# Kernel tuning notes

Measured on AMD Instinct MI355X. Metric: run time of the kernel, lower is better.

Reference implementation:

```python
import jax, jax.numpy as jnp
import numpy as np

EPS = 1e-5

def rmsnorm(x):
    # BitLinear pre-norm (no learnable scale), per BitNet b1.58 reference impl
    return x * jax.lax.rsqrt(jnp.mean(x * x, axis=-1, keepdims=True) + EPS)

def act_quant(x):
    # per-token absmax 8-bit quantization with straight-through estimator
    scale = 127.0 / jnp.clip(jnp.max(jnp.abs(x), axis=-1, keepdims=True), 1e-5)
    q = jnp.clip(jnp.round(x * scale), -128.0, 127.0) / scale
    return x + jax.lax.stop_gradient(q - x)

def weight_quant(w):
    # absmean ternary quantization {-1,0,1} with STE
    scale = 1.0 / jnp.clip(jnp.mean(jnp.abs(w)), 1e-5)
    q = jnp.clip(jnp.round(w * scale), -1.0, 1.0) / scale
    return w + jax.lax.stop_gradient(q - w)

def bitlinear(x, w, b):
    # x: [b, s, d_in], w: [d_out, d_in] (torch Linear layout), b: [d_out]
    xq = act_quant(rmsnorm(x))
    wq = weight_quant(w)
    return jnp.einsum('bsd,fd->bsf', xq, wq) + b

def setup_inputs() -> dict:
    key = jax.random.key(0)
    k0, k1, k2 = jax.random.split(key, 3)
    B, S, D, F = 2, 8192, 1024, 4096  # inner_dim = dim * mult = 4096
    x = jax.random.normal(k0, (B, S, D), dtype=jnp.float32)
    w1 = jax.random.normal(k1, (F, D), dtype=jnp.float32) * (1.0 / np.sqrt(D))
    b1 = jnp.zeros((F,), dtype=jnp.float32)
    w2 = jax.random.normal(k2, (D, F), dtype=jnp.float32) * (1.0 / np.sqrt(F))
    b2 = jnp.zeros((D,), dtype=jnp.float32)
    return {"x": x, "w1": w1, "b1": b1, "w2": w2, "b2": b2}

def reference(x, w1, b1, w2, b2):
    h = bitlinear(x, w1, b1)
    h = jax.nn.gelu(h, approximate=False)  # nn.GELU() default is exact
    # post_act_ln=False -> no LayerNorm; dropout p=0.0 -> identity
    return bitlinear(h, w2, b2)
```

## Files before the change

### kernel.cpp

```cpp
#include <hip/hip_runtime.h>
#include <hip/hip_bf16.h>
#include <stdint.h>

typedef int i32x4 __attribute__((ext_vector_type(4)));

__device__ __forceinline__ float blo(unsigned int u) {
  unsigned int v = u << 16; float f; __builtin_memcpy(&f, &v, 4); return f;
}
__device__ __forceinline__ float bhi(unsigned int u) {
  unsigned int v = u & 0xffff0000u; float f; __builtin_memcpy(&f, &v, 4); return f;
}
__device__ __forceinline__ int pack4q(float a, float b, float c, float d, float qm) {
  int i0 = (int)rintf(a * qm) & 255;
  int i1 = (int)rintf(b * qm) & 255;
  int i2 = (int)rintf(c * qm) & 255;
  int i3 = (int)rintf(d * qm) & 255;
  return i0 | (i1 << 8) | (i2 << 16) | (i3 << 24);
}

__device__ __forceinline__ float fast_gelu(float v) {
  float u = v * 0.70710678118654752f;
  float s = fabsf(u);
  float den = fmaf(0.3275911f, s, 1.0f);
  float t;
  asm("v_rcp_f32 %0, %1" : "=v"(t) : "v"(den));
  float p = t * fmaf(t, fmaf(t, fmaf(t, fmaf(t, 1.061405429f, -1.453152027f),
                                     1.421413741f), -0.284496736f), 0.254829592f);
  float e = fmaf(-p, __expf(-u * u), 1.0f);
  float er = copysignf(e, u);
  return 0.5f * v * (1.0f + er);
}

__global__ void k_reduce_abs2(const float* __restrict__ w1, const float* __restrict__ w2,
                              long n4, float* __restrict__ partials) {
  const int half = gridDim.x >> 1;
  const float* w = (blockIdx.x < half) ? w1 : w2;
  int b = (blockIdx.x < half) ? blockIdx.x : blockIdx.x - half;
  const float4* wv = (const float4*)w;
  float s = 0.0f;
  long stride = (long)half * blockDim.x;
  for (long i = (long)b * blockDim.x + threadIdx.x; i < n4; i += stride) {
    float4 v = wv[i];
    s += fabsf(v.x) + fabsf(v.y) + fabsf(v.z) + fabsf(v.w);
  }
  #pragma unroll
  for (int off = 32; off; off >>= 1) s += __shfl_down(s, off);
  __shared__ float sw[4];
  if ((threadIdx.x & 63) == 0) sw[threadIdx.x >> 6] = s;
  __syncthreads();
  if (threadIdx.x == 0) partials[blockIdx.x] = sw[0] + sw[1] + sw[2] + sw[3];
}

__global__ void k_quant_w2(const float* __restrict__ w1, char* __restrict__ wq1,
                           const float* __restrict__ w2, char* __restrict__ wq2,
                           long n4, const float* __restrict__ partials,
                           float* __restrict__ scales, float invW) {
  const int half = gridDim.x >> 1;
  const bool first = blockIdx.x < half;
  int t = threadIdx.x;
  float p = partials[(first ? 0 : 256) + t];
  #pragma unroll
  for (int off = 32; off; off >>= 1) p += __shfl_down(p, off);
  __shared__ float a[4];
  if ((t & 63) == 0) a[t >> 6] = p;
  __syncthreads();
  float sc = fmaxf((a[0] + a[1] + a[2] + a[3]) * invW, 1e-5f);
  if (t == 0 && (blockIdx.x == 0 || blockIdx.x == half)) scales[first ? 0 : 1] = sc;
  float s = 1.0f / sc;
  const float* w = first ? w1 : w2;
  char* wq = first ? wq1 : wq2;
  int b = first ? blockIdx.x : blockIdx.x - half;
  const float4* wv = (const float4*)w;
  int* qv = (int*)wq;
  long stride = (long)half * blockDim.x;
  for (long i = (long)b * blockDim.x + t; i < n4; i += stride) {
    float4 v = wv[i];
    int b0 = (int)fminf(fmaxf(rintf(v.x * s), -1.0f), 1.0f) & 255;
    int b1 = (int)fminf(fmaxf(rintf(v.y * s), -1.0f), 1.0f) & 255;
    int b2 = (int)fminf(fmaxf(rintf(v.z * s), -1.0f), 1.0f) & 255;
    int b3 = (int)fminf(fmaxf(rintf(v.w * s), -1.0f), 1.0f) & 255;
    qv[i] = b0 | (b1 << 8) | (b2 << 16) | (b3 << 24);
  }
}

__global__ void k_actq_x(const float* __restrict__ x, char* __restrict__ xq,
                         float* __restrict__ alpha) {
  const int D = 1024;
  size_t t = blockIdx.x;
  int tid = threadIdx.x;
  const float4* row = (const float4*)(x + t * (size_t)D);
  float4 v = row[tid];
  float ss = v.x*v.x + v.y*v.y + v.z*v.z + v.w*v.w;
  float am = fmaxf(fmaxf(fabsf(v.x), fabsf(v.y)), fmaxf(fabsf(v.z), fabsf(v.w)));
  #pragma unroll
  for (int off = 32; off; off >>= 1) {
    ss += __shfl_down(ss, off);
    am = fmaxf(am, __shfl_down(am, off));
  }
  __shared__ float s_ss[4], s_am[4];
  if ((tid & 63) == 0) { s_ss[tid >> 6] = ss; s_am[tid >> 6] = am; }
  __syncthreads();
  ss = s_ss[0] + s_ss[1] + s_ss[2] + s_ss[3];
  am = fmaxf(fmaxf(s_am[0], s_am[1]), fmaxf(s_am[2], s_am[3]));
  float rms = rsqrtf(ss * (1.0f / D) + 1e-5f);
  float a   = fmaxf(am * rms, 1e-5f);
  float qs  = 127.0f / a;
  if (tid == 0) alpha[t] = a * (1.0f / 127.0f);
  int b0 = (int)fminf(fmaxf(rintf((v.x * rms) * qs), -128.0f), 127.0f) & 255;
  int b1 = (int)fminf(fmaxf(rintf((v.y * rms) * qs), -128.0f), 127.0f) & 255;
  int b2 = (int)fminf(fmaxf(rintf((v.z * rms) * qs), -128.0f), 127.0f) & 255;
  int b3 = (int)fminf(fmaxf(rintf((v.w * rms) * qs), -128.0f), 127.0f) & 255;
  ((int*)xq)[t * 256 + tid] = b0 | (b1 << 8) | (b2 << 16) | (b3 << 24);
}

__global__ void k_actq_h(__hip_bfloat16* __restrict__ h, float* __restrict__ alpha) {
  const int F = 4096;
  size_t t = blockIdx.x;
  int tid = threadIdx.x;
  char* rb = (char*)(h + t * (size_t)F);
  const uint4* row = (const uint4*)rb;
  uint4 u0 = row[tid], u1 = row[tid + 256];
  unsigned int uu[8] = {u0.x, u0.y, u0.z, u0.w, u1.x, u1.y, u1.z, u1.w};
  float ss = 0.0f, am = 0.0f;
  #pragma unroll
  for (int i = 0; i < 8; i++) {
    float f0 = blo(uu[i]), f1 = bhi(uu[i]);
    ss += f0 * f0 + f1 * f1;
    am = fmaxf(am, fmaxf(fabsf(f0), fabsf(f1)));
  }
  #pragma unroll
  for (int off = 32; off; off >>= 1) {
    ss += __shfl_down(ss, off);
    am = fmaxf(am, __shfl_down(am, off));
  }
  __shared__ float s_ss[4], s_am[4];
  if ((tid & 63) == 0) { s_ss[tid >> 6] = ss; s_am[tid >> 6] = am; }
  __syncthreads();
  ss = s_ss[0] + s_ss[1] + s_ss[2] + s_ss[3];
  am = fmaxf(fmaxf(s_am[0], s_am[1]), fmaxf(s_am[2], s_am[3]));
  float rms = rsqrtf(ss * (1.0f / F) + 1e-5f);
  float a   = fmaxf(am * rms, 1e-5f);
  float qm  = rms * (127.0f / a);
  if (tid == 0) alpha[t] = a * (1.0f / 127.0f);
  uint2 w0, w1;
  w0.x = (unsigned)pack4q(blo(uu[0]), bhi(uu[0]), blo(uu[1]), bhi(uu[1]), qm);
  w0.y = (unsigned)pack4q(blo(uu[2]), bhi(uu[2]), blo(uu[3]), bhi(uu[3]), qm);
  w1.x = (unsigned)pack4q(blo(uu[4]), bhi(uu[4]), blo(uu[5]), bhi(uu[5]), qm);
  w1.y = (unsigned)pack4q(blo(uu[6]), bhi(uu[6]), blo(uu[7]), bhi(uu[7]), qm);
  *(uint2*)(rb + 8 * tid) = w0;
  *(uint2*)(rb + 2048 + 8 * tid) = w1;
}

#define GLD16(GP, LP) __builtin_amdgcn_global_load_lds( \
    (__attribute__((address_space(1))) void*)(GP), \
    (__attribute__((address_space(3))) void*)(LP), 16, 0, 0)
#define VMCNT4 asm volatile("s_waitcnt vmcnt(4)" ::: "memory")
#define VMCNT0 asm volatile("s_waitcnt vmcnt(0)" ::: "memory")
#define LGKM0  do { asm volatile("s_waitcnt lgkmcnt(0)" ::: "memory"); __builtin_amdgcn_sched_barrier(0); } while(0)

template<int EPI>
__global__ __launch_bounds__(512, 2) void k_gemm_i8(
    const char* __restrict__ A, int lda,
    const char* __restrict__ B,
    const float* __restrict__ bias, const float* __restrict__ alpha,
    const float* __restrict__ scales, int which,
    void* __restrict__ Cout, int N, int K, int lgnbx)
{
  __shared__ __align__(16) char lA[3 * 16384];
  __shared__ __align__(16) char lB[3 * 16384];
  const int tid = threadIdx.x, lane = tid & 63, wid = tid >> 6;
  const int wm = wid >> 2, wn = wid & 3;
  const int nwg = gridDim.x, bid = blockIdx.x;
  const int swz = (bid & 7) * (nwg >> 3) + (bid >> 3);
  const int bx = swz & ((1 << lgnbx) - 1), by = swz >> lgnbx;
  const int m0 = by * 256, n0 = bx * 256;
  const int NT = K >> 6;

  const int srow = tid >> 2, slot = tid & 3;
  const int sswz = (slot ^ ((srow >> 1) & 3)) * 16;
  const char* gA0 = A + (size_t)(m0 +       srow) * lda + sswz;
  const char* gA1 = A + (size_t)(m0 + 128 + srow) * lda + sswz;
  const char* gB0 = B + (size_t)(n0 +       srow) * K   + sswz;
  const char* gB1 = B + (size_t)(n0 + 128 + srow) * K   + sswz;
  const int ldst = srow * 64 + slot * 16;

  const int lr = lane & 15;
  const int kx = ((lane >> 4) ^ ((lane >> 1) & 3)) * 16;
  const int aoff = (wm * 128 + lr) * 64 + kx;
  const int boff = (wn * 64  + lr) * 64 + kx;

  GLD16(gA0,      lA + ldst);
  GLD16(gA1,      lA + 8192 + ldst);
  GLD16(gB0,      lB + ldst);
  GLD16(gB1,      lB + 8192 + ldst);
  GLD16(gA0 + 64, lA + 16384 + ldst);
  GLD16(gA1 + 64, lA + 16384 + 8192 + ldst);
  GLD16(gB0 + 64, lB + 16384 + ldst);
  GLD16(gB1 + 64, lB + 16384 + 8192 + ldst);

  i32x4 acc[8][4] = {};
  int cur = 0, nx1 = 1, nx2 = 2;
  for (int t = 0; t < NT; ++t) {
    const bool pf = (t + 2 < NT);
    if (t + 1 < NT) { VMCNT4; } else { VMCNT0; }
    __builtin_amdgcn_s_barrier();
    const char* pa = lA + cur * 16384 + aoff;
    const char* pb = lB + cur * 16384 + boff;
    i32x4 av[4], bv[4];
    #pragma unroll
    for (int j = 0; j < 4; ++j) av[j] = *(const i32x4*)(pa + j * 1024);
    #pragma unroll
    for (int n = 0; n < 4; ++n) bv[n] = *(const i32x4*)(pb + n * 1024);
    if (pf) {
      GLD16(gA0 + 64 * (t + 2), lA + nx2 * 16384 + ldst);
      GLD16(gA1 + 64 * (t + 2), lA + nx2 * 16384 + 8192 + ldst);
    }
    __builtin_amdgcn_s_barrier();
    LGKM0;
    __builtin_amdgcn_s_setprio(1);
    #pragma unroll
    for (int j = 0; j < 4; ++j)
      #pragma unroll
      for (int n = 0; n < 4; ++n)
        acc[j][n] = __builtin_amdgcn_mfma_i32_16x16x64_i8(av[j], bv[n], acc[j][n], 0, 0, 0);
    __builtin_amdgcn_s_setprio(0);
    __builtin_amdgcn_s_barrier();
    #pragma unroll
    for (int j = 0; j < 4; ++j) av[j] = *(const i32x4*)(pa + (4 + j) * 1024);
    if (pf) {
      GLD16(gB0 + 64 * (t + 2), lB + nx2 * 16384 + ldst);
      GLD16(gB1 + 64 * (t + 2), lB + nx2 * 16384 + 8192 + ldst);
    }
    LGKM0;
    __builtin_amdgcn_s_setprio(1);
    #pragma unroll
    for (int j = 0; j < 4; ++j)
      #pragma unroll
      for (int n = 0; n < 4; ++n)
        acc[4 + j][n] = __builtin_amdgcn_mfma_i32_16x16x64_i8(av[j], bv[n], acc[4 + j][n], 0, 0, 0);
    __builtin_amdgcn_s_setprio(0);
    int tmp = cur; cur = nx1; nx1 = nx2; nx2 = tmp;
  }

  const float wdq = scales[which];
  const int lq4 = (lane >> 4) * 4;
  #pragma unroll
  for (int m = 0; m < 8; ++m) {
    const int rowb = m0 + wm * 128 + m * 16 + lq4;
    float al[4];
    #pragma unroll
    for (int q = 0; q < 4; ++q) al[q] = alpha[rowb + q] * wdq;
    #pragma unroll
    for (int n = 0; n < 4; ++n) {
      const int col = n0 + wn * 64 + n * 16 + lr;
      const float bb = bias[col];
      #pragma unroll
      for (int q = 0; q < 4; ++q) {
        float v = (float)acc[m][n][q] * al[q] + bb;
        if constexpr (EPI == 0) {
          ((__hip_bfloat16*)Cout)[(size_t)(rowb + q) * N + col] = __float2bfloat16(fast_gelu(v));
        } else {
          ((float*)Cout)[(size_t)(rowb + q) * N + col] = v;
        }
      }
    }
  }
}

extern "C" void kernel_launch(void* const* d_in, const int* in_sizes, int n_in,
                              void* d_out, int out_size, void* d_ws, size_t ws_size,
                              hipStream_t stream) {
  const float* x  = (const float*)d_in[0];
  const float* w1 = (const float*)d_in[1];
  const float* b1 = (const float*)d_in[2];
  const float* w2 = (const float*)d_in[3];
  const float* b2 = (const float*)d_in[4];
  const int  F = in_sizes[2];
  const int  D = in_sizes[4];
  const long T = (long)in_sizes[0] / D;
  const long nW = (long)F * D;

  char* ws = (char*)d_ws;
  float* partials = (float*)ws;
  float* scales   = partials + 512;
  float* alpha1 = (float*)(ws + 4096);
  float* alpha2 = alpha1 + T;
  size_t off = 4096 + 2 * (size_t)T * sizeof(float);
  off = (off + 255) & ~(size_t)255;
  char* w1q = ws + off; off += (size_t)nW;
  char* w2q = ws + off; off += (size_t)nW;
  char* xq  = ws + off; off += (size_t)T * D;
  off = (off + 255) & ~(size_t)255;
  __hip_bfloat16* h = (__hip_bfloat16*)(ws + off); off += (size_t)T * F * 2;
  if (ws_size < off) return;

  float invW = (float)(1.0 / (double)nW);
  k_reduce_abs2<<<512, 256, 0, stream>>>(w1, w2, nW / 4, partials);
  k_quant_w2<<<4096, 256, 0, stream>>>(w1, w1q, w2, w2q, nW / 4, partials, scales, invW);
  k_actq_x<<<(unsigned)T, 256, 0, stream>>>(x, xq, alpha1);

  dim3 g1((unsigned)((T / 256) * (F / 256)));
  k_gemm_i8<0><<<g1, 512, 0, stream>>>(xq, D, w1q, b1, alpha1, scales, 0,
                                       h, F, D, __builtin_ctz(F / 256));

  k_actq_h<<<(unsigned)T, 256, 0, stream>>>(h, alpha2);

  dim3 g2((unsigned)((T / 256) * (D / 256)));
  k_gemm_i8<1><<<g2, 512, 0, stream>>>((const char*)h, F * 2, w2q, b2, alpha2, scales, 1,
                                       (float*)d_out, D, F, __builtin_ctz(D / 256));
}
```

Baseline: 242.9 us.

## Split GEMM1 into dedicated 128x256 tile kernel with higher occupancy

The first int8 GEMM gets its own kernel with a 128x256 output tile in place of 256x256. Each warp now holds a 4x4 accumulator block, and launch bounds are raised to allow 4 workgroups per CU. The K-step is split into two MFMA halves with the B prefetch spread between them. The aim is better latency hiding and more CUs busy on the GELU-producing GEMM, at the cost of less data reuse per tile and more barriers.

```diff
diff --git a/kernel.cpp b/kernel.cpp
--- a/kernel.cpp
+++ b/kernel.cpp
@@ -154,17 +154,114 @@
 #define GLD16(GP, LP) __builtin_amdgcn_global_load_lds( \
     (__attribute__((address_space(1))) void*)(GP), \
     (__attribute__((address_space(3))) void*)(LP), 16, 0, 0)
+#define VMCNT3 asm volatile("s_waitcnt vmcnt(3)" ::: "memory")
 #define VMCNT4 asm volatile("s_waitcnt vmcnt(4)" ::: "memory")
 #define VMCNT0 asm volatile("s_waitcnt vmcnt(0)" ::: "memory")
 #define LGKM0  do { asm volatile("s_waitcnt lgkmcnt(0)" ::: "memory"); __builtin_amdgcn_sched_barrier(0); } while(0)
 
-template<int EPI>
-__global__ __launch_bounds__(512, 2) void k_gemm_i8(
+__global__ __launch_bounds__(512, 4) void k_gemm1(
+    const char* __restrict__ A, const char* __restrict__ B,
+    const float* __restrict__ bias, const float* __restrict__ alpha,
+    const float* __restrict__ scales,
+    __hip_bfloat16* __restrict__ H, int N, int K, int lgnbx)
+{
+  __shared__ __align__(16) char lA[3 * 8192];
+  __shared__ __align__(16) char lB[3 * 16384];
+  const int tid = threadIdx.x, lane = tid & 63, wid = tid >> 6;
+  const int wm = wid >> 2, wn = wid & 3;
+  const int nwg = gridDim.x, bid = blockIdx.x;
+  const int swz = (bid & 7) * (nwg >> 3) + (bid >> 3);
+  const int bx = swz & ((1 << lgnbx) - 1), by = swz >> lgnbx;
+  const int m0 = by * 128, n0 = bx * 256;
+  const int NT = K >> 6;
+
+  const int srow = tid >> 2, slot = tid & 3;
+  const int sswz = (slot ^ ((srow >> 1) & 3)) * 16;
+  const char* gA0 = A + (size_t)(m0 +       srow) * K + sswz;
+  const char* gB0 = B + (size_t)(n0 +       srow) * K + sswz;
+  const char* gB1 = B + (size_t)(n0 + 128 + srow) * K + sswz;
+  const int ldst = srow * 64 + slot * 16;
+
+  const int lr = lane & 15;
+  const int kx = ((lane >> 4) ^ ((lane >> 1) & 3)) * 16;
+  const int aoff = (wm * 64 + lr) * 64 + kx;
+  const int boff = (wn * 64 + lr) * 64 + kx;
+
+  GLD16(gA0,      lA + ldst);
+  GLD16(gB0,      lB + ldst);
+  GLD16(gB1,      lB + 8192 + ldst);
+  GLD16(gA0 + 64, lA + 8192 + ldst);
+  GLD16(gB0 + 64, lB + 16384 + ldst);
+  GLD16(gB1 + 64, lB + 16384 + 8192 + ldst);
+
+  i32x4 acc[4][4] = {};
+  int cur = 0, nx1 = 1, nx2 = 2;
+  for (int t = 0; t < NT; ++t) {
+    const bool pf = (t + 2 < NT);
+    if (t + 1 < NT) { VMCNT3; } else { VMCNT0; }
+    __builtin_amdgcn_s_barrier();
+    const char* pa = lA + cur * 8192 + aoff;
+    const char* pb = lB + cur * 16384 + boff;
+    i32x4 av[4], bv[4];
+    av[0] = *(const i32x4*)(pa);
+    av[1] = *(const i32x4*)(pa + 1024);
+    #pragma unroll
+    for (int n = 0; n < 4; ++n) bv[n] = *(const i32x4*)(pb + n * 1024);
+    if (pf) {
+      GLD16(gA0 + 64 * (t + 2), lA + nx2 * 8192 + ldst);
+      GLD16(gB0 + 64 * (t + 2), lB + nx2 * 16384 + ldst);
+    }
+    __builtin_amdgcn_s_barrier();
+    LGKM0;
+    __builtin_amdgcn_s_setprio(1);
+    #pragma unroll
+    for (int j = 0; j < 2; ++j)
+      #pragma unroll
+      for (int n = 0; n < 4; ++n)
+        acc[j][n] = __builtin_amdgcn_mfma_i32_16x16x64_i8(av[j], bv[n], acc[j][n], 0, 0, 0);
+    __builtin_amdgcn_s_setprio(0);
+    __builtin_amdgcn_s_barrier();
+    av[2] = *(const i32x4*)(pa + 2048);
+    av[3] = *(const i32x4*)(pa + 3072);
+    if (pf) GLD16(gB1 + 64 * (t + 2), lB + nx2 * 16384 + 8192 + ldst);
+    LGKM0;
+    __builtin_amdgcn_s_setprio(1);
+    #pragma unroll
+    for (int j = 2; j < 4; ++j)
+      #pragma unroll
+      for (int n = 0; n < 4; ++n)
+        acc[j][n] = __builtin_amdgcn_mfma_i32_16x16x64_i8(av[j], bv[n], acc[j][n], 0, 0, 0);
+    __builtin_amdgcn_s_setprio(0);
+    int tmp = cur; cur = nx1; nx1 = nx2; nx2 = tmp;
+  }
+
+  const float wdq = scales[0];
+  const int lq4 = (lane >> 4) * 4;
+  #pragma unroll
+  for (int m = 0; m < 4; ++m) {
+    const int rowb = m0 + wm * 64 + m * 16 + lq4;
+    float al[4];
+    #pragma unroll
+    for (int q = 0; q < 4; ++q) al[q] = alpha[rowb + q] * wdq;
+    #pragma unroll
+    for (int n = 0; n < 4; ++n) {
+      const int col = n0 + wn * 64 + n * 16 + lr;
+      const float bb = bias[col];
+      #pragma unroll
+      for (int q = 0; q < 4; ++q) {
+        float v = (float)acc[m][n][q] * al[q] + bb;
+        H[(size_t)(rowb + q) * N + col] = __float2bfloat16(fast_gelu(v));
+      }
+    }
+  }
+}
+
+__global__ __launch_bounds__(512, 2) void k_gemm2(
     const char* __restrict__ A, int lda,
     const char* __restrict__ B,
     const float* __restrict__ bias, const float* __restrict__ alpha,
-    const float* __restrict__ scales, int which,
-    void* __restrict__ Cout, int N, int K, int lgnbx)
+    const float* __restrict__ scales,
+    float* __restrict__ Out, int N, int K, int lgnbx)
 {
   __shared__ __align__(16) char lA[3 * 16384];
   __shared__ __align__(16) char lB[3 * 16384];
@@ -242,7 +339,7 @@
     int tmp = cur; cur = nx1; nx1 = nx2; nx2 = tmp;
   }
 
-  const float wdq = scales[which];
+  const float wdq = scales[1];
   const int lq4 = (lane >> 4) * 4;
   #pragma unroll
   for (int m = 0; m < 8; ++m) {
@@ -255,14 +352,8 @@
       const int col = n0 + wn * 64 + n * 16 + lr;
       const float bb = bias[col];
       #pragma unroll
-      for (int q = 0; q < 4; ++q) {
-        float v = (float)acc[m][n][q] * al[q] + bb;
-        if constexpr (EPI == 0) {
-          ((__hip_bfloat16*)Cout)[(size_t)(rowb + q) * N + col] = __float2bfloat16(fast_gelu(v));
-        } else {
-          ((float*)Cout)[(size_t)(rowb + q) * N + col] = v;
-        }
-      }
+      for (int q = 0; q < 4; ++q)
+        Out[(size_t)(rowb + q) * N + col] = (float)acc[m][n][q] * al[q] + bb;
     }
   }
 }
@@ -299,13 +390,13 @@
   k_quant_w2<<<4096, 256, 0, stream>>>(w1, w1q, w2, w2q, nW / 4, partials, scales, invW);
   k_actq_x<<<(unsigned)T, 256, 0, stream>>>(x, xq, alpha1);
 
-  dim3 g1((unsigned)((T / 256) * (F / 256)));
-  k_gemm_i8<0><<<g1, 512, 0, stream>>>(xq, D, w1q, b1, alpha1, scales, 0,
-                                       h, F, D, __builtin_ctz(F / 256));
+  dim3 g1((unsigned)((T / 128) * (F / 256)));
+  k_gemm1<<<g1, 512, 0, stream>>>(xq, w1q, b1, alpha1, scales, h, F, D,
+                                  __builtin_ctz(F / 256));
 
   k_actq_h<<<(unsigned)T, 256, 0, stream>>>(h, alpha2);
 
   dim3 g2((unsigned)((T / 256) * (D / 256)));
-  k_gemm_i8<1><<<g2, 512, 0, stream>>>((const char*)h, F * 2, w2q, b2, alpha2, scales, 1,
-                                       (float*)d_out, D, F, __builtin_ctz(D / 256));
-}
+  k_gemm2<<<g2, 512, 0, stream>>>((const char*)h, F * 2, w2q, b2, alpha2, scales,
+                                  (float*)d_out, D, F, __builtin_ctz(D / 256));
+}
```

Result: no change. 243.8 us (+0.4%).
